# Kernel optimization log

Hardware: AMD Instinct MI355X
Metric: run time of the kernel (lower is better)

Reference implementation:

```python
import jax, jax.numpy as jnp
import numpy as np

DIM = 1024
HEADS = 16
HEAD_DIM = DIM // HEADS
EPS = 1e-5


def setup_inputs() -> dict:
    key = jax.random.key(0)
    ks = jax.random.split(key, 4)
    N, L = 4, 2048
    x = jax.random.normal(ks[0], (N, L, DIM), dtype=jnp.float32)
    # causal mask: True means masked (strictly upper triangle)
    attn_mask = jnp.triu(jnp.ones((L, L), dtype=jnp.bool_), k=1)[None, None, :, :]
    w_qkv = jax.random.normal(ks[1], (3 * DIM, DIM), dtype=jnp.float32) * (DIM ** -0.5)
    w_proj = jax.random.normal(ks[2], (DIM, DIM), dtype=jnp.float32) * (DIM ** -0.5)
    b_proj = jnp.zeros((DIM,), dtype=jnp.float32)
    q_gamma = jnp.ones((HEAD_DIM,), dtype=jnp.float32)
    q_beta = jnp.zeros((HEAD_DIM,), dtype=jnp.float32)
    k_gamma = jnp.ones((HEAD_DIM,), dtype=jnp.float32)
    k_beta = jnp.zeros((HEAD_DIM,), dtype=jnp.float32)
    return {"x": x, "attn_mask": attn_mask, "w_qkv": w_qkv, "w_proj": w_proj,
            "b_proj": b_proj, "q_gamma": q_gamma, "q_beta": q_beta,
            "k_gamma": k_gamma, "k_beta": k_beta}


def _layernorm(h, gamma, beta):
    mu = jnp.mean(h, axis=-1, keepdims=True)
    var = jnp.mean(jnp.square(h - mu), axis=-1, keepdims=True)
    return (h - mu) * jax.lax.rsqrt(var + EPS) * gamma + beta


def reference(x, attn_mask, w_qkv, w_proj, b_proj, q_gamma, q_beta, k_gamma, k_beta):
    N, L, D = x.shape
    H, hd = HEADS, HEAD_DIM
    scale = hd ** -0.5
    qkv = jnp.einsum('nld,ed->nle', x, w_qkv)  # [N, L, 3D]
    qkv = qkv.reshape(N, L, 3, H, hd).transpose(2, 0, 3, 1, 4)  # [3, N, H, L, hd]
    q, k, v = qkv[0], qkv[1], qkv[2]
    q = _layernorm(q, q_gamma, q_beta)
    k = _layernorm(k, k_gamma, k_beta)
    scores = jnp.einsum('nhqd,nhkd->nhqk', q * scale, k)
    scores = scores + jnp.where(attn_mask, -jnp.inf, 0.0).astype(scores.dtype)
    attn = jax.nn.softmax(scores, axis=-1)
    out = jnp.einsum('nhqk,nhkd->nhqd', attn, v)  # [N, H, L, hd]
    out = out.transpose(0, 2, 1, 3).reshape(N, L, D)
    return jnp.einsum('nld,ed->nle', out, w_proj) + b_proj
```

## Files before the change

### kernel.cpp

```cpp
#include <hip/hip_runtime.h>


using f16x8 = __attribute__((ext_vector_type(8))) _Float16;
using f16x4 = __attribute__((ext_vector_type(4))) _Float16;
using f16x2 = __attribute__((ext_vector_type(2))) _Float16;
using f32x4 = __attribute__((ext_vector_type(4))) float;
using f32x16 = __attribute__((ext_vector_type(16))) float;
using u32x4 = __attribute__((ext_vector_type(4))) unsigned int;

#define MFMA16(a, b, c) __builtin_amdgcn_mfma_f32_16x16x32_f16(a, b, c, 0, 0, 0)
#define MFMA32(a, b, c) __builtin_amdgcn_mfma_f32_32x32x16_f16(a, b, c, 0, 0, 0)

__device__ __forceinline__ void gload_lds16(const void* g, void* l) {
  __builtin_amdgcn_global_load_lds(
      (const __attribute__((address_space(1))) unsigned int*)g,
      (__attribute__((address_space(3))) unsigned int*)l, 16, 0, 0);
}

__device__ __forceinline__ float dot2acc(unsigned int pk, float c) {
#if __has_builtin(__builtin_amdgcn_fdot2)
  const f16x2 ones = {(_Float16)1.f, (_Float16)1.f};
  return __builtin_amdgcn_fdot2(__builtin_bit_cast(f16x2, pk), ones, c, false);
#else
  f16x2 v = __builtin_bit_cast(f16x2, pk);
  return c + (float)v[0] + (float)v[1];
#endif
}

__global__ __launch_bounds__(256) void f32_to_f16_kernel(
    const float* __restrict__ in, _Float16* __restrict__ out, int n) {
  int i = (blockIdx.x * 256 + threadIdx.x) * 8;
  if (i >= n) return;
  float4 a = *(const float4*)(in + i);
  float4 b = *(const float4*)(in + i + 4);
  f16x8 o;
  o[0] = (_Float16)a.x; o[1] = (_Float16)a.y; o[2] = (_Float16)a.z; o[3] = (_Float16)a.w;
  o[4] = (_Float16)b.x; o[5] = (_Float16)b.y; o[6] = (_Float16)b.z; o[7] = (_Float16)b.w;
  *(f16x8*)(out + i) = o;
}

template <int MODE>
__global__ __launch_bounds__(256) void gemm_bt(
    const _Float16* __restrict__ A, const _Float16* __restrict__ B,
    void* __restrict__ Cout, const float* __restrict__ bias,
    const float* __restrict__ qg, const float* __restrict__ qb,
    const float* __restrict__ kg, const float* __restrict__ kb,
    int M, int N, int K) {
  __shared__ __align__(16) _Float16 As[2][128 * 32];
  __shared__ __align__(16) _Float16 Bs[2][128 * 32];
  const int tid = threadIdx.x;
  const int w = tid >> 6, lane = tid & 63;
  const int c = lane & 15, g = lane >> 4;
  const long mbase = (long)blockIdx.x * 128;
  const long nbase = (long)blockIdx.y * 128;
  const int wm = (w >> 1) * 64, wn = (w & 1) * 64;
  const int srow = w * 32 + (lane >> 2);
  const int scol = ((lane & 3) ^ ((lane >> 3) & 3)) * 8;
  const int sg = (g ^ ((c >> 1) & 3)) * 8;

#define GSTAGE(buf, kt_)                                                      \
  {                                                                           \
    const int kk_ = (kt_) * 32;                                               \
    gload_lds16(A + (mbase + srow) * K + kk_ + scol, &As[buf][w * 1024]);     \
    gload_lds16(A + (mbase + srow + 16) * K + kk_ + scol,                     \
                &As[buf][w * 1024 + 512]);                                    \
    gload_lds16(B + (nbase + srow) * K + kk_ + scol, &Bs[buf][w * 1024]);     \
    gload_lds16(B + (nbase + srow + 16) * K + kk_ + scol,                     \
                &Bs[buf][w * 1024 + 512]);                                    \
  }

  f32x4 acc[4][4];
#pragma unroll
  for (int i = 0; i < 4; ++i)
#pragma unroll
    for (int j = 0; j < 4; ++j) acc[i][j] = f32x4{0.f, 0.f, 0.f, 0.f};

  const int nk = K >> 5;
  GSTAGE(0, 0);
  for (int kt = 0; kt < nk; ++kt) {
    const int cur = kt & 1;
    __syncthreads();
    if (kt + 1 < nk) GSTAGE(cur ^ 1, kt + 1);
    f16x8 af[4], bfr[4];
#pragma unroll
    for (int mt = 0; mt < 4; ++mt)
      af[mt] = *(const f16x8*)(&As[cur][(wm + mt * 16 + c) * 32 + sg]);
#pragma unroll
    for (int nt = 0; nt < 4; ++nt)
      bfr[nt] = *(const f16x8*)(&Bs[cur][(wn + nt * 16 + c) * 32 + sg]);
    __builtin_amdgcn_s_setprio(1);
#pragma unroll
    for (int mt = 0; mt < 4; ++mt)
#pragma unroll
      for (int nt = 0; nt < 4; ++nt)
        acc[mt][nt] = MFMA16(af[mt], bfr[nt], acc[mt][nt]);
    __builtin_amdgcn_s_setprio(0);
  }
#undef GSTAGE

  if constexpr (MODE == 1) {
    const int region = (int)(nbase >> 10);
    if (region < 2) {
      const float* gamma = region ? kg : qg;
      const float* beta = region ? kb : qb;
      float gam[4], bet[4];
#pragma unroll
      for (int nt = 0; nt < 4; ++nt) {
        gam[nt] = gamma[nt * 16 + c];
        bet[nt] = beta[nt * 16 + c];
      }
      const float sc = region ? 1.f : 0.1803368801111204f;
#pragma unroll
      for (int mt = 0; mt < 4; ++mt)
#pragma unroll
        for (int r = 0; r < 4; ++r) {
          float s1 = 0.f, s2 = 0.f;
#pragma unroll
          for (int nt = 0; nt < 4; ++nt) {
            const float v = acc[mt][nt][r];
            s1 += v;
            s2 += v * v;
          }
#pragma unroll
          for (int msk = 1; msk < 16; msk <<= 1) {
            s1 += __shfl_xor(s1, msk);
            s2 += __shfl_xor(s2, msk);
          }
          const float mu = s1 * 0.015625f;
          const float rstd = rsqrtf(s2 * 0.015625f - mu * mu + 1e-5f);
#pragma unroll
          for (int nt = 0; nt < 4; ++nt)
            acc[mt][nt][r] =
                ((acc[mt][nt][r] - mu) * rstd * gam[nt] + bet[nt]) * sc;
        }
    }
#pragma unroll
    for (int nt = 0; nt < 4; ++nt) {
      const long col = nbase + wn + nt * 16 + c;
#pragma unroll
      for (int mt = 0; mt < 4; ++mt)
#pragma unroll
        for (int r = 0; r < 4; ++r) {
          const long row = mbase + wm + mt * 16 + g * 4 + r;
          ((_Float16*)Cout)[row * N + col] = (_Float16)acc[mt][nt][r];
        }
    }
  } else {
#pragma unroll
    for (int nt = 0; nt < 4; ++nt) {
      const long col = nbase + wn + nt * 16 + c;
      const float bv = bias ? bias[col] : 0.f;
#pragma unroll
      for (int mt = 0; mt < 4; ++mt)
#pragma unroll
        for (int r = 0; r < 4; ++r) {
          const long row = mbase + wm + mt * 16 + g * 4 + r;
          ((float*)Cout)[row * N + col] = acc[mt][nt][r] + bv;
        }
    }
  }
}

__global__ __launch_bounds__(256) void transpose_v_kernel(
    const _Float16* __restrict__ qkv, _Float16* __restrict__ Vt) {
  __shared__ __align__(16) _Float16 tile[64][80];
  const int nh = blockIdx.y;
  const long n = nh >> 4;
  const int h = nh & 15;
  const long lbase = (long)blockIdx.x * 64;
  const int t = threadIdx.x;
#pragma unroll
  for (int r = 0; r < 2; ++r) {
    const int l = (t + r * 256) >> 3;
    const int cc = (t & 7) * 8;
    f16x8 v = *(const f16x8*)(qkv + (n * 2048 + lbase + l) * 3072 + 2048 + h * 64 + cc);
    *(f16x8*)&tile[l][cc] = v;
  }
  __syncthreads();
  const int d = t >> 2, q = t & 3;
  f16x8 o0, o1;
#pragma unroll
  for (int i = 0; i < 8; ++i) {
    o0[i] = tile[q * 16 + i][d];
    o1[i] = tile[q * 16 + 8 + i][d];
  }
  _Float16* dst = Vt + ((long)nh * 64 + d) * 2048 + lbase + q * 16;
  *(f16x8*)dst = o0;
  *(f16x8*)(dst + 8) = o1;
}

__global__ __launch_bounds__(256) void attn_kernel(
    const _Float16* __restrict__ qkv, const _Float16* __restrict__ Vt,
    _Float16* __restrict__ Ob) {
  __shared__ __align__(16) _Float16 Ks[2][64 * 64];
  __shared__ __align__(16) _Float16 Vs[2][64 * 64];
  const int w = threadIdx.x >> 6;
  const int lane = threadIdx.x & 63;
  const int c5 = lane & 31;
  const int hi = lane >> 5;
  const int nh = blockIdx.x;
  const long n = nh >> 4;
  const int h = nh & 15;
  const int qtile = 15 - blockIdx.y;
  const int qlo_blk = qtile * 128;
  const int qlo = qlo_blk + w * 32;
  const int qrow = qlo + c5;

  const _Float16* Qp = qkv + n * 2048 * 3072 + h * 64;
  const _Float16* Kq = Qp + 1024;
  const _Float16* Vp = Vt + (long)nh * 64 * 2048;

  const int sr8 = lane >> 3;
  const int scol = ((lane & 7) ^ sr8) * 8;

  const int nkv_blk = (qlo_blk + 191) >> 6;
  const int nkv_w = (qlo + 95) >> 6;

#define STAGE(buf, kv)                                                        \
  {                                                                           \
    const int kb_ = (kv) * 64;                                                \
    _Pragma("unroll") for (int i = 0; i < 2; ++i) {                           \
      const int idx = w * 2 + i;                                              \
      const int row = idx * 8 + sr8;                                          \
      gload_lds16(Kq + (long)(kb_ + row) * 3072 + scol, &Ks[buf][idx * 512]); \
      gload_lds16(Vp + (long)row * 2048 + kb_ + scol, &Vs[buf][idx * 512]);   \
    }                                                                         \
  }

  f16x8 qf[4];
#pragma unroll
  for (int dc = 0; dc < 4; ++dc)
    qf[dc] = *(const f16x8*)(Qp + (long)qrow * 3072 + dc * 16 + hi * 8);

  f32x16 negM;
#pragma unroll
  for (int r = 0; r < 16; ++r) negM[r] = -12.0f;

  f32x16 acc[2];
#pragma unroll
  for (int db = 0; db < 2; ++db)
#pragma unroll
    for (int r = 0; r < 16; ++r) acc[db][r] = 0.f;
  float ls = 0.f;

  STAGE(0, 0);

  const int swr = c5 & 7;

  for (int kv = 0; kv < nkv_blk; ++kv) {
    const int cur = kv & 1;
    __syncthreads();
    if (kv + 1 < nkv_blk) STAGE(cur ^ 1, kv + 1);

    if (kv < nkv_w) {
      const int kbase = kv * 64;
      const _Float16* Kb = Ks[cur];
      const _Float16* Vb = Vs[cur];
      f32x16 s0, s1;
      __builtin_amdgcn_s_setprio(1);
      {
        const int b = hi ^ swr;
        f16x8 kf0 = *(const f16x8*)(Kb + c5 * 64 + b * 8);
        f16x8 kf1 = *(const f16x8*)(Kb + (32 + c5) * 64 + b * 8);
        s0 = MFMA32(kf0, qf[0], negM);
        s1 = MFMA32(kf1, qf[0], negM);
      }
#pragma unroll
      for (int dc = 1; dc < 4; ++dc) {
        const int b = (dc * 2 + hi) ^ swr;
        f16x8 kf0 = *(const f16x8*)(Kb + c5 * 64 + b * 8);
        f16x8 kf1 = *(const f16x8*)(Kb + (32 + c5) * 64 + b * 8);
        s0 = MFMA32(kf0, qf[dc], s0);
        s1 = MFMA32(kf1, qf[dc], s1);
      }
      __builtin_amdgcn_s_setprio(0);
      if (kbase + 63 > qlo) {
#pragma unroll
        for (int r = 0; r < 16; ++r) {
          const int mv = (r & 3) + 8 * (r >> 2) + 4 * hi;
          if (kbase + mv > qrow) s0[r] = -1e30f;
          if (kbase + 32 + mv > qrow) s1[r] = -1e30f;
        }
      }
#pragma unroll
      for (int r = 0; r < 16; ++r) {
        s0[r] = exp2f(s0[r]);
        s1[r] = exp2f(s1[r]);
      }
      unsigned int pk0[4][2], pk1[4][2];
#pragma unroll
      for (int r2 = 0; r2 < 4; ++r2)
#pragma unroll
        for (int p = 0; p < 2; ++p) {
          pk0[r2][p] = __builtin_bit_cast(
              unsigned int,
              __builtin_amdgcn_cvt_pkrtz(s0[4 * r2 + 2 * p], s0[4 * r2 + 2 * p + 1]));
          pk1[r2][p] = __builtin_bit_cast(
              unsigned int,
              __builtin_amdgcn_cvt_pkrtz(s1[4 * r2 + 2 * p], s1[4 * r2 + 2 * p + 1]));
        }
#pragma unroll
      for (int r2 = 0; r2 < 4; ++r2)
#pragma unroll
        for (int p = 0; p < 2; ++p) {
          ls = dot2acc(pk0[r2][p], ls);
          ls = dot2acc(pk1[r2][p], ls);
        }
      f16x8 pB[4];
#pragma unroll
      for (int kk = 0; kk < 4; ++kk) {
        const int rx = (kk & 1) * 2;
        unsigned int x0 = (kk < 2) ? pk0[rx][0] : pk1[rx][0];
        unsigned int y0 = (kk < 2) ? pk0[rx + 1][0] : pk1[rx + 1][0];
        unsigned int x1 = (kk < 2) ? pk0[rx][1] : pk1[rx][1];
        unsigned int y1 = (kk < 2) ? pk0[rx + 1][1] : pk1[rx + 1][1];
        asm("v_permlane32_swap_b32 %0, %1" : "+v"(x0), "+v"(y0));
        asm("v_permlane32_swap_b32 %0, %1" : "+v"(x1), "+v"(y1));
        pB[kk] = __builtin_bit_cast(f16x8, u32x4{x0, x1, y0, y1});
      }
      __builtin_amdgcn_s_setprio(1);
#pragma unroll
      for (int db = 0; db < 2; ++db)
#pragma unroll
        for (int kk = 0; kk < 4; ++kk) {
          const int rowd = db * 32 + c5;
          const int bb = (kk * 2 + hi) ^ swr;
          f16x8 vf = *(const f16x8*)(Vb + rowd * 64 + bb * 8);
          acc[db] = MFMA32(vf, pB[kk], acc[db]);
        }
      __builtin_amdgcn_s_setprio(0);
    }
  }
  const float lsr = ls + __shfl_xor(ls, 32);
  const float inv = 1.f / lsr;
  _Float16* ob = Ob + ((long)(n * 2048) + qrow) * 1024 + h * 64 + 4 * hi;
#pragma unroll
  for (int db = 0; db < 2; ++db)
#pragma unroll
    for (int r2 = 0; r2 < 4; ++r2) {
      f16x4 o;
#pragma unroll
      for (int j = 0; j < 4; ++j)
        o[j] = (_Float16)(acc[db][4 * r2 + j] * inv);
      *(f16x4*)(ob + db * 32 + 8 * r2) = o;
    }
#undef STAGE
}

extern "C" void kernel_launch(void* const* d_in, const int* in_sizes, int n_in,
                              void* d_out, int out_size, void* d_ws, size_t ws_size,
                              hipStream_t stream) {
  const float* x = (const float*)d_in[0];
  const float* w_qkv = (const float*)d_in[2];
  const float* w_proj = (const float*)d_in[3];
  const float* b_proj = (const float*)d_in[4];
  const float* qg = (const float*)d_in[5];
  const float* qb = (const float*)d_in[6];
  const float* kg = (const float*)d_in[7];
  const float* kb = (const float*)d_in[8];

  char* ws = (char*)d_ws;
  _Float16* xb     = (_Float16*)(ws + 0);
  _Float16* wqkvb  = (_Float16*)(ws + 16777216);
  _Float16* wprojb = (_Float16*)(ws + 23068672);
  _Float16* qkvh   = (_Float16*)(ws + 25165824);
  _Float16* Vt     = (_Float16*)(ws + 75497472);
  _Float16* Ob     = xb;

  f32_to_f16_kernel<<<4096, 256, 0, stream>>>(x, xb, 8388608);
  f32_to_f16_kernel<<<1536, 256, 0, stream>>>(w_qkv, wqkvb, 3145728);
  f32_to_f16_kernel<<<512, 256, 0, stream>>>(w_proj, wprojb, 1048576);

  gemm_bt<1><<<dim3(64, 24), 256, 0, stream>>>(xb, wqkvb, qkvh, nullptr,
                                               qg, qb, kg, kb, 8192, 3072, 1024);
  transpose_v_kernel<<<dim3(32, 64), 256, 0, stream>>>(qkvh, Vt);
  attn_kernel<<<dim3(64, 16), 256, 0, stream>>>(qkvh, Vt, Ob);
  gemm_bt<0><<<dim3(64, 8), 256, 0, stream>>>(Ob, wprojb, d_out, b_proj,
                                              nullptr, nullptr, nullptr, nullptr,
                                              8192, 1024, 1024);
}
```

Measured before the change: 210.3 us.

## Deepen GEMM prefetch with explicit waitcnt/barriers and unroll attention loop by two

The GEMM main loop now prefetches two k-tiles ahead, using explicit vmcnt waits and split barriers so the next global-to-LDS load is issued only after the current fragments are read into registers, with precomputed LDS pointers. The attention kernel is unrolled by two with a static buffer index, so LDS addresses become compile-time offsets from precomputed base pointers, and it gets a launch_bounds occupancy hint of 4. The aim is to hide global load latency and cut address arithmetic, at the cost of fragile hand-written wait counts and possible register pressure from the occupancy hint.

```diff
diff --git a/kernel.cpp b/kernel.cpp
--- a/kernel.cpp
+++ b/kernel.cpp
@@ -57,6 +57,8 @@
   const int srow = w * 32 + (lane >> 2);
   const int scol = ((lane & 3) ^ ((lane >> 3) & 3)) * 8;
   const int sg = (g ^ ((c >> 1) & 3)) * 8;
+  const char* pAr = (const char*)As + (wm + c) * 64 + sg * 2;
+  const char* pBr = (const char*)Bs + (wn + c) * 64 + sg * 2;
 
 #define GSTAGE(buf, kt_)                                                      \
   {                                                                           \
@@ -69,6 +71,33 @@
                 &Bs[buf][w * 1024 + 512]);                                    \
   }
 
+#define GPHASE(BUF, t_)                                                       \
+  {                                                                           \
+    if ((t_) + 1 < nk) {                                                      \
+      asm volatile("s_waitcnt vmcnt(4)" ::: "memory");                        \
+    } else {                                                                  \
+      asm volatile("s_waitcnt vmcnt(0)" ::: "memory");                        \
+    }                                                                         \
+    __builtin_amdgcn_sched_barrier(0);                                        \
+    __builtin_amdgcn_s_barrier();                                             \
+    __builtin_amdgcn_sched_barrier(0);                                        \
+    f16x8 af[4], bfr[4];                                                      \
+    _Pragma("unroll") for (int mt = 0; mt < 4; ++mt)                          \
+        af[mt] = *(const f16x8*)(pAr + (BUF) * 8192 + mt * 1024);             \
+    _Pragma("unroll") for (int nt = 0; nt < 4; ++nt)                          \
+        bfr[nt] = *(const f16x8*)(pBr + (BUF) * 8192 + nt * 1024);            \
+    asm volatile("s_waitcnt lgkmcnt(0)" ::: "memory");                        \
+    __builtin_amdgcn_sched_barrier(0);                                        \
+    __builtin_amdgcn_s_barrier();                                             \
+    __builtin_amdgcn_sched_barrier(0);                                        \
+    if ((t_) + 2 < nk) GSTAGE(BUF, (t_) + 2);                                 \
+    __builtin_amdgcn_s_setprio(1);                                            \
+    _Pragma("unroll") for (int mt = 0; mt < 4; ++mt)                          \
+        _Pragma("unroll") for (int nt = 0; nt < 4; ++nt)                      \
+            acc[mt][nt] = MFMA16(af[mt], bfr[nt], acc[mt][nt]);               \
+    __builtin_amdgcn_s_setprio(0);                                            \
+  }
+
   f32x4 acc[4][4];
 #pragma unroll
   for (int i = 0; i < 4; ++i)
@@ -77,25 +106,12 @@
 
   const int nk = K >> 5;
   GSTAGE(0, 0);
-  for (int kt = 0; kt < nk; ++kt) {
-    const int cur = kt & 1;
-    __syncthreads();
-    if (kt + 1 < nk) GSTAGE(cur ^ 1, kt + 1);
-    f16x8 af[4], bfr[4];
-#pragma unroll
-    for (int mt = 0; mt < 4; ++mt)
-      af[mt] = *(const f16x8*)(&As[cur][(wm + mt * 16 + c) * 32 + sg]);
-#pragma unroll
-    for (int nt = 0; nt < 4; ++nt)
-      bfr[nt] = *(const f16x8*)(&Bs[cur][(wn + nt * 16 + c) * 32 + sg]);
-    __builtin_amdgcn_s_setprio(1);
-#pragma unroll
-    for (int mt = 0; mt < 4; ++mt)
-#pragma unroll
-      for (int nt = 0; nt < 4; ++nt)
-        acc[mt][nt] = MFMA16(af[mt], bfr[nt], acc[mt][nt]);
-    __builtin_amdgcn_s_setprio(0);
-  }
+  GSTAGE(1, 1);
+  for (int kt = 0; kt < nk; kt += 2) {
+    GPHASE(0, kt);
+    GPHASE(1, kt + 1);
+  }
+#undef GPHASE
 #undef GSTAGE
 
   if constexpr (MODE == 1) {
@@ -189,11 +205,10 @@
   *(f16x8*)(dst + 8) = o1;
 }
 
-__global__ __launch_bounds__(256) void attn_kernel(
+__global__ __launch_bounds__(256, 4) void attn_kernel(
     const _Float16* __restrict__ qkv, const _Float16* __restrict__ Vt,
     _Float16* __restrict__ Ob) {
-  __shared__ __align__(16) _Float16 Ks[2][64 * 64];
-  __shared__ __align__(16) _Float16 Vs[2][64 * 64];
+  __shared__ __align__(16) char lds[32768];
   const int w = threadIdx.x >> 6;
   const int lane = threadIdx.x & 63;
   const int c5 = lane & 31;
@@ -216,15 +231,17 @@
   const int nkv_blk = (qlo_blk + 191) >> 6;
   const int nkv_w = (qlo + 95) >> 6;
 
-#define STAGE(buf, kv)                                                        \
-  {                                                                           \
-    const int kb_ = (kv) * 64;                                                \
-    _Pragma("unroll") for (int i = 0; i < 2; ++i) {                           \
-      const int idx = w * 2 + i;                                              \
-      const int row = idx * 8 + sr8;                                          \
-      gload_lds16(Kq + (long)(kb_ + row) * 3072 + scol, &Ks[buf][idx * 512]); \
-      gload_lds16(Vp + (long)row * 2048 + kb_ + scol, &Vs[buf][idx * 512]);   \
-    }                                                                         \
+#define STAGE(BUF, kv_)                                                        \
+  {                                                                            \
+    const int kb_ = (kv_) * 64;                                                \
+    _Pragma("unroll") for (int i = 0; i < 2; ++i) {                            \
+      const int idx = w * 2 + i;                                               \
+      const int row = idx * 8 + sr8;                                           \
+      gload_lds16(Kq + (long)(kb_ + row) * 3072 + scol,                        \
+                  lds + (BUF) * 8192 + idx * 1024);                            \
+      gload_lds16(Vp + (long)row * 2048 + kb_ + scol,                          \
+                  lds + 16384 + (BUF) * 8192 + idx * 1024);                    \
+    }                                                                          \
   }
 
   f16x8 qf[4];
@@ -243,94 +260,89 @@
     for (int r = 0; r < 16; ++r) acc[db][r] = 0.f;
   float ls = 0.f;
 
+  const int swr = c5 & 7;
+  const char* Lb[4];
+#pragma unroll
+  for (int j = 0; j < 4; ++j)
+    Lb[j] = lds + c5 * 128 + (((j * 2 + hi) ^ swr) << 4);
+
+#define COMPUTE(BUF, kv_)                                                      \
+  {                                                                            \
+    const int kbase = (kv_) * 64;                                              \
+    f32x16 s0, s1;                                                             \
+    __builtin_amdgcn_s_setprio(1);                                             \
+    {                                                                          \
+      f16x8 kf0 = *(const f16x8*)(Lb[0] + (BUF) * 8192);                       \
+      f16x8 kf1 = *(const f16x8*)(Lb[0] + (BUF) * 8192 + 4096);                \
+      s0 = MFMA32(kf0, qf[0], negM);                                           \
+      s1 = MFMA32(kf1, qf[0], negM);                                           \
+    }                                                                          \
+    _Pragma("unroll") for (int dc = 1; dc < 4; ++dc) {                         \
+      f16x8 kf0 = *(const f16x8*)(Lb[dc] + (BUF) * 8192);                      \
+      f16x8 kf1 = *(const f16x8*)(Lb[dc] + (BUF) * 8192 + 4096);               \
+      s0 = MFMA32(kf0, qf[dc], s0);                                            \
+      s1 = MFMA32(kf1, qf[dc], s1);                                            \
+    }                                                                          \
+    __builtin_amdgcn_s_setprio(0);                                             \
+    if (kbase + 63 > qlo) {                                                    \
+      _Pragma("unroll") for (int r = 0; r < 16; ++r) {                         \
+        const int mv = (r & 3) + 8 * (r >> 2) + 4 * hi;                        \
+        if (kbase + mv > qrow) s0[r] = -1e30f;                                 \
+        if (kbase + 32 + mv > qrow) s1[r] = -1e30f;                            \
+      }                                                                        \
+    }                                                                          \
+    _Pragma("unroll") for (int r = 0; r < 16; ++r) {                           \
+      s0[r] = exp2f(s0[r]);                                                    \
+      s1[r] = exp2f(s1[r]);                                                    \
+    }                                                                          \
+    unsigned int pk0[4][2], pk1[4][2];                                         \
+    _Pragma("unroll") for (int r2 = 0; r2 < 4; ++r2)                           \
+        _Pragma("unroll") for (int p = 0; p < 2; ++p) {                        \
+      pk0[r2][p] = __builtin_bit_cast(                                         \
+          unsigned int, __builtin_amdgcn_cvt_pkrtz(s0[4 * r2 + 2 * p],         \
+                                                   s0[4 * r2 + 2 * p + 1]));   \
+      pk1[r2][p] = __builtin_bit_cast(                                         \
+          unsigned int, __builtin_amdgcn_cvt_pkrtz(s1[4 * r2 + 2 * p],         \
+                                                   s1[4 * r2 + 2 * p + 1]));   \
+    }                                                                          \
+    _Pragma("unroll") for (int r2 = 0; r2 < 4; ++r2)                           \
+        _Pragma("unroll") for (int p = 0; p < 2; ++p) {                        \
+      ls = dot2acc(pk0[r2][p], ls);                                            \
+      ls = dot2acc(pk1[r2][p], ls);                                            \
+    }                                                                          \
+    f16x8 pB[4];                                                               \
+    _Pragma("unroll") for (int kk = 0; kk < 4; ++kk) {                         \
+      const int rx = (kk & 1) * 2;                                             \
+      unsigned int x0 = (kk < 2) ? pk0[rx][0] : pk1[rx][0];                    \
+      unsigned int y0 = (kk < 2) ? pk0[rx + 1][0] : pk1[rx + 1][0];            \
+      unsigned int x1 = (kk < 2) ? pk0[rx][1] : pk1[rx][1];                    \
+      unsigned int y1 = (kk < 2) ? pk0[rx + 1][1] : pk1[rx + 1][1];            \
+      asm("v_permlane32_swap_b32 %0, %1" : "+v"(x0), "+v"(y0));                \
+      asm("v_permlane32_swap_b32 %0, %1" : "+v"(x1), "+v"(y1));                \
+      pB[kk] = __builtin_bit_cast(f16x8, u32x4{x0, x1, y0, y1});               \
+    }                                                                          \
+    __builtin_amdgcn_s_setprio(1);                                             \
+    _Pragma("unroll") for (int db = 0; db < 2; ++db)                           \
+        _Pragma("unroll") for (int kk = 0; kk < 4; ++kk) {                     \
+      f16x8 vf = *(const f16x8*)(Lb[kk] + 16384 + (BUF) * 8192 + db * 4096);   \
+      acc[db] = MFMA32(vf, pB[kk], acc[db]);                                   \
+    }                                                                          \
+    __builtin_amdgcn_s_setprio(0);                                             \
+  }
+
   STAGE(0, 0);
-
-  const int swr = c5 & 7;
-
-  for (int kv = 0; kv < nkv_blk; ++kv) {
-    const int cur = kv & 1;
+  for (int kv = 0; kv < nkv_blk; kv += 2) {
     __syncthreads();
-    if (kv + 1 < nkv_blk) STAGE(cur ^ 1, kv + 1);
-
-    if (kv < nkv_w) {
-      const int kbase = kv * 64;
-      const _Float16* Kb = Ks[cur];
-      const _Float16* Vb = Vs[cur];
-      f32x16 s0, s1;
-      __builtin_amdgcn_s_setprio(1);
-      {
-        const int b = hi ^ swr;
-        f16x8 kf0 = *(const f16x8*)(Kb + c5 * 64 + b * 8);
-        f16x8 kf1 = *(const f16x8*)(Kb + (32 + c5) * 64 + b * 8);
-        s0 = MFMA32(kf0, qf[0], negM);
-        s1 = MFMA32(kf1, qf[0], negM);
-      }
-#pragma unroll
-      for (int dc = 1; dc < 4; ++dc) {
-        const int b = (dc * 2 + hi) ^ swr;
-        f16x8 kf0 = *(const f16x8*)(Kb + c5 * 64 + b * 8);
-        f16x8 kf1 = *(const f16x8*)(Kb + (32 + c5) * 64 + b * 8);
-        s0 = MFMA32(kf0, qf[dc], s0);
-        s1 = MFMA32(kf1, qf[dc], s1);
-      }
-      __builtin_amdgcn_s_setprio(0);
-      if (kbase + 63 > qlo) {
-#pragma unroll
-        for (int r = 0; r < 16; ++r) {
-          const int mv = (r & 3) + 8 * (r >> 2) + 4 * hi;
-          if (kbase + mv > qrow) s0[r] = -1e30f;
-          if (kbase + 32 + mv > qrow) s1[r] = -1e30f;
-        }
-      }
-#pragma unroll
-      for (int r = 0; r < 16; ++r) {
-        s0[r] = exp2f(s0[r]);
-        s1[r] = exp2f(s1[r]);
-      }
-      unsigned int pk0[4][2], pk1[4][2];
-#pragma unroll
-      for (int r2 = 0; r2 < 4; ++r2)
-#pragma unroll
-        for (int p = 0; p < 2; ++p) {
-          pk0[r2][p] = __builtin_bit_cast(
-              unsigned int,
-              __builtin_amdgcn_cvt_pkrtz(s0[4 * r2 + 2 * p], s0[4 * r2 + 2 * p + 1]));
-          pk1[r2][p] = __builtin_bit_cast(
-              unsigned int,
-              __builtin_amdgcn_cvt_pkrtz(s1[4 * r2 + 2 * p], s1[4 * r2 + 2 * p + 1]));
-        }
-#pragma unroll
-      for (int r2 = 0; r2 < 4; ++r2)
-#pragma unroll
-        for (int p = 0; p < 2; ++p) {
-          ls = dot2acc(pk0[r2][p], ls);
-          ls = dot2acc(pk1[r2][p], ls);
-        }
-      f16x8 pB[4];
-#pragma unroll
-      for (int kk = 0; kk < 4; ++kk) {
-        const int rx = (kk & 1) * 2;
-        unsigned int x0 = (kk < 2) ? pk0[rx][0] : pk1[rx][0];
-        unsigned int y0 = (kk < 2) ? pk0[rx + 1][0] : pk1[rx + 1][0];
-        unsigned int x1 = (kk < 2) ? pk0[rx][1] : pk1[rx][1];
-        unsigned int y1 = (kk < 2) ? pk0[rx + 1][1] : pk1[rx + 1][1];
-        asm("v_permlane32_swap_b32 %0, %1" : "+v"(x0), "+v"(y0));
-        asm("v_permlane32_swap_b32 %0, %1" : "+v"(x1), "+v"(y1));
-        pB[kk] = __builtin_bit_cast(f16x8, u32x4{x0, x1, y0, y1});
-      }
-      __builtin_amdgcn_s_setprio(1);
-#pragma unroll
-      for (int db = 0; db < 2; ++db)
-#pragma unroll
-        for (int kk = 0; kk < 4; ++kk) {
-          const int rowd = db * 32 + c5;
-          const int bb = (kk * 2 + hi) ^ swr;
-          f16x8 vf = *(const f16x8*)(Vb + rowd * 64 + bb * 8);
-          acc[db] = MFMA32(vf, pB[kk], acc[db]);
-        }
-      __builtin_amdgcn_s_setprio(0);
-    }
-  }
+    if (kv + 1 < nkv_blk) STAGE(1, kv + 1);
+    if (kv < nkv_w) COMPUTE(0, kv);
+    if (kv + 1 >= nkv_blk) break;
+    __syncthreads();
+    if (kv + 2 < nkv_blk) STAGE(0, kv + 2);
+    if (kv + 1 < nkv_w) COMPUTE(1, kv + 1);
+  }
+#undef COMPUTE
+#undef STAGE
+
   const float lsr = ls + __shfl_xor(ls, 32);
   const float inv = 1.f / lsr;
   _Float16* ob = Ob + ((long)(n * 2048) + qrow) * 1024 + h * 64 + 4 * hi;
@@ -344,7 +356,6 @@
         o[j] = (_Float16)(acc[db][4 * r2 + j] * inv);
       *(f16x4*)(ob + db * 32 + 8 * r2) = o;
     }
-#undef STAGE
 }
 
 extern "C" void kernel_launch(void* const* d_in, const int* in_sizes, int n_in,
```

After: 197.6 us. 1.06x faster.
